# Performance work log

Hardware: AMD Instinct MI355X
Metric: run time of the kernel (lower is better)

## Reference

```python
import jax, jax.numpy as jnp
import numpy as np

V_IN, V_OUT = 128, 128
E_IN, E_OUT = 64, 64
H, L, D = 256, 2, 2
DEC_H = D * L * H  # 1024
S_IN, B, S_OUT = 128, 512, 64


def _lstm_step(h, c, x, W_ih, W_hh, b):
    # PyTorch gate order: i, f, g, o
    gates = x @ W_ih.T + h @ W_hh.T + b
    i, f, g, o = jnp.split(gates, 4, axis=-1)
    c = jax.nn.sigmoid(f) * c + jax.nn.sigmoid(i) * jnp.tanh(g)
    h = jax.nn.sigmoid(o) * jnp.tanh(c)
    return h, c


def _run_lstm_dir(x_seq, W_ih, W_hh, b, reverse):
    # x_seq: [S, B, in]; returns hidden sequence [S, B, H], final (h, c)
    Bsz = x_seq.shape[1]
    Hd = W_hh.shape[1]
    init = (jnp.zeros((Bsz, Hd), x_seq.dtype), jnp.zeros((Bsz, Hd), x_seq.dtype))

    def step(carry, x):
        h, c = _lstm_step(carry[0], carry[1], x, W_ih, W_hh, b)
        return (h, c), h

    (hf, cf), hs = jax.lax.scan(step, init, x_seq, reverse=reverse)
    return hs, hf, cf


def setup_inputs() -> dict:
    key = jax.random.key(0)
    ks = jax.random.split(key, 20)
    s = 0.05
    inp = {}
    inp["input_tokens"] = jax.random.randint(ks[0], (S_IN, B), 0, V_IN, dtype=jnp.int32)
    inp["output_tokens"] = jax.random.randint(ks[1], (B, S_OUT), 0, V_OUT, dtype=jnp.int32)
    inp["in_emb"] = jax.random.normal(ks[2], (V_IN, E_IN), jnp.float32) * s
    # encoder layer 0: input E_IN; layer 1: input D*H. Leading dim 2 = directions.
    inp["enc_W_ih0"] = jax.random.normal(ks[3], (2, 4 * H, E_IN), jnp.float32) * s
    inp["enc_W_hh0"] = jax.random.normal(ks[4], (2, 4 * H, H), jnp.float32) * s
    inp["enc_b0"] = jax.random.normal(ks[5], (2, 4 * H), jnp.float32) * s
    inp["enc_W_ih1"] = jax.random.normal(ks[6], (2, 4 * H, D * H), jnp.float32) * s
    inp["enc_W_hh1"] = jax.random.normal(ks[7], (2, 4 * H, H), jnp.float32) * s
    inp["enc_b1"] = jax.random.normal(ks[8], (2, 4 * H), jnp.float32) * s
    inp["out_emb"] = jax.random.normal(ks[9], (V_OUT, E_OUT), jnp.float32) * s
    inp["dec_W_ih"] = jax.random.normal(ks[10], (4 * DEC_H, E_OUT), jnp.float32) * s
    inp["dec_W_hh"] = jax.random.normal(ks[11], (4 * DEC_H, DEC_H), jnp.float32) * s
    inp["dec_b"] = jax.random.normal(ks[12], (4 * DEC_H,), jnp.float32) * s
    inp["proj_W"] = jax.random.normal(ks[13], (V_OUT, DEC_H), jnp.float32) * s
    inp["proj_b"] = jax.random.normal(ks[14], (V_OUT,), jnp.float32) * s
    return inp


def reference(input_tokens, output_tokens, in_emb,
              enc_W_ih0, enc_W_hh0, enc_b0,
              enc_W_ih1, enc_W_hh1, enc_b1,
              out_emb, dec_W_ih, dec_W_hh, dec_b, proj_W, proj_b):
    # ---- encoder: 2-layer bidirectional LSTM over [S_in, B] ----
    x = in_emb[input_tokens]  # [S, B, E_IN]
    h_list, c_list = [], []
    for W_ih, W_hh, b in ((enc_W_ih0, enc_W_hh0, enc_b0),
                          (enc_W_ih1, enc_W_hh1, enc_b1)):
        hs_f, hf, cf = _run_lstm_dir(x, W_ih[0], W_hh[0], b[0], False)
        hs_b, hb, cb = _run_lstm_dir(x, W_ih[1], W_hh[1], b[1], True)
        x = jnp.concatenate([hs_f, hs_b], axis=-1)  # [S, B, 2H]
        h_list += [hf, hb]
        c_list += [cf, cb]
    Bsz = x.shape[1]
    # PyTorch h_n order: (l0_fwd, l0_bwd, l1_fwd, l1_bwd) -> swapaxes+reshape
    h0 = jnp.stack(h_list, axis=1).reshape(Bsz, -1)  # [B, D*L*H]
    c0 = jnp.stack(c_list, axis=1).reshape(Bsz, -1)

    # ---- decoder: teacher-forced LSTMCell loop ----
    tok_in = output_tokens[:, :-1].T   # [T-1, B]
    tok_next = output_tokens[:, 1:].T  # [T-1, B]

    def step(carry, toks):
        h, c = carry
        t_in, t_next = toks
        e = out_emb[t_in]                                 # [B, E_OUT]
        h, c = _lstm_step(h, c, e, dec_W_ih, dec_W_hh, dec_b)
        logits = c @ proj_W.T + proj_b                    # NOTE: proj on CELL, as in source
        greedy = jnp.argmax(logits, axis=1)
        lp = jax.nn.log_softmax(logits, axis=-1)
        logp = jnp.take_along_axis(lp, t_next[:, None], axis=1)[:, 0]
        return (h, c), (greedy, logp)

    _, (decoded_tokens, log_probs) = jax.lax.scan(step, (h0, c0), (tok_in, tok_next))
    cum_log_probs = jnp.sum(log_probs, axis=0)  # [B]
    return decoded_tokens, cum_log_probs
```

## Files before the change

kernel.cpp:

```cpp
#include <hip/hip_runtime.h>
#include <math.h>

#define B 512
#define S_IN 128
#define S_OUT 64
#define T_DEC 63

#define O_H0   0
#define O_H1   524288
#define O_C    1048576
#define O_BAR  1572864
#define O_HS0  1572868
#define O_P1   (O_HS0 + 33554432)
#define D_HT0  O_HS0
#define D_HT1  (O_HS0 + 524288)
#define D_CT0  (O_HS0 + 1048576)
#define D_CT1  (O_HS0 + 1572864)
#define D_PWT  (O_HS0 + 2097152)

template<int MODE>
__global__ __launch_bounds__(256)
void enc_step(const float* __restrict__ Wih, const float* __restrict__ Whh,
              const float* __restrict__ bias, const int* __restrict__ tok,
              const float* __restrict__ emb, const float* __restrict__ seqin,
              const float* __restrict__ h_in, float* __restrict__ h_out,
              float* __restrict__ c_st, float* __restrict__ seqout,
              const float* __restrict__ p1, int t)
{
    constexpr int KE = (MODE==0) ? 64 : (MODE==2 ? 512 : 0);
    constexpr int K  = KE + 256;
    constexpr int NK = K/16;

    const int dir   = blockIdx.z;
    const int t_eff = dir ? (S_IN-1-t) : t;
    const int hseg  = (MODE==0) ? dir*256 : 512 + dir*256;

    const float* Wih_d = Wih + (size_t)dir*1024*KE;
    const float* Whh_d = Whh + (size_t)dir*1024*256;
    const float* b_d   = bias + dir*1024;

    __shared__ float As[16][64];
    __shared__ float Bs[16][64];

    const int tid = threadIdx.x;
    const int bm0 = blockIdx.x*64;
    const int bn0 = blockIdx.y*64;

    const int la_m  = tid >> 2;
    const int la_k  = (tid & 3) << 2;
    const int a_row = bm0 + la_m;

    const int lb_n = tid >> 2;
    const int lb_k = (tid & 3) << 2;
    const int n_g  = bn0 + lb_n;
    const int b_j  = (n_g & 3)*256 + (n_g >> 2);

    int tokidx = 0;
    if (MODE==0) tokidx = tok[t_eff*B + a_row];

    const int tm = (tid >> 4) << 2;
    const int tn = (tid & 15) << 2;

    float acc[4][4] = {};

    auto loadA = [&](int kt) -> float4 {
        int k = kt*16 + la_k;
        if (MODE==0) {
            if (k < 64) return *(const float4*)&emb[(size_t)tokidx*64 + k];
            return *(const float4*)&h_in[(size_t)a_row*1024 + hseg + (k-64)];
        } else if (MODE==2) {
            if (k < 512) return *(const float4*)&seqin[((size_t)t_eff*B + a_row)*512 + k];
            return *(const float4*)&h_in[(size_t)a_row*1024 + hseg + (k-512)];
        } else {
            return *(const float4*)&h_in[(size_t)a_row*1024 + hseg + k];
        }
    };
    auto loadB = [&](int kt) -> float4 {
        int k = kt*16 + lb_k;
        if (KE && k < KE) return *(const float4*)&Wih_d[(size_t)b_j*KE + k];
        return *(const float4*)&Whh_d[(size_t)b_j*256 + (k-KE)];
    };

    float4 aR = loadA(0), bR = loadB(0);
    for (int kt=0; kt<NK; ++kt) {
        __syncthreads();
        As[la_k+0][la_m]=aR.x; As[la_k+1][la_m]=aR.y; As[la_k+2][la_m]=aR.z; As[la_k+3][la_m]=aR.w;
        Bs[lb_k+0][lb_n]=bR.x; Bs[lb_k+1][lb_n]=bR.y; Bs[lb_k+2][lb_n]=bR.z; Bs[lb_k+3][lb_n]=bR.w;
        __syncthreads();
        if (kt+1 < NK) { aR = loadA(kt+1); bR = loadB(kt+1); }
        #pragma unroll
        for (int k=0;k<16;k++){
            const float4 a = *(const float4*)&As[k][tm];
            const float4 b = *(const float4*)&Bs[k][tn];
            acc[0][0]+=a.x*b.x; acc[0][1]+=a.x*b.y; acc[0][2]+=a.x*b.z; acc[0][3]+=a.x*b.w;
            acc[1][0]+=a.y*b.x; acc[1][1]+=a.y*b.y; acc[1][2]+=a.y*b.z; acc[1][3]+=a.y*b.w;
            acc[2][0]+=a.z*b.x; acc[2][1]+=a.z*b.y; acc[2][2]+=a.z*b.z; acc[2][3]+=a.z*b.w;
            acc[3][0]+=a.w*b.x; acc[3][1]+=a.w*b.y; acc[3][2]+=a.w*b.z; acc[3][3]+=a.w*b.w;
        }
    }

    const int jh = (bn0 + tn) >> 2;
    const float bi = b_d[0*256 + jh];
    const float bf = b_d[1*256 + jh];
    const float bg = b_d[2*256 + jh];
    const float bo = b_d[3*256 + jh];
    #pragma unroll
    for (int i=0;i<4;i++){
        const int brow = bm0 + tm + i;
        float xi = acc[i][0] + bi;
        float xf = acc[i][1] + bf;
        float xg = acc[i][2] + bg;
        float xo = acc[i][3] + bo;
        if (MODE==1) {
            const float4 pv = *(const float4*)&p1[((size_t)dir*512 + brow)*1024 + bn0 + tn];
            xi += pv.x; xf += pv.y; xg += pv.z; xo += pv.w;
        }
        float ig = 1.f/(1.f+expf(-xi));
        float fg = 1.f/(1.f+expf(-xf));
        float gg = tanhf(xg);
        float og = 1.f/(1.f+expf(-xo));
        size_t ci = (size_t)brow*1024 + hseg + jh;
        float cn = fg*c_st[ci] + ig*gg;
        float hn = og*tanhf(cn);
        c_st[ci]  = cn;
        h_out[ci] = hn;
        if (MODE==0) seqout[((size_t)t_eff*B + brow)*512 + dir*256 + jh] = hn;
    }
}

__global__ __launch_bounds__(128)
void gemm_p1(const float* __restrict__ Wih, const float* __restrict__ hs0,
             float* __restrict__ p1out, int s0)
{
    constexpr int NK = 512/16;
    const int dir = blockIdx.z;

    __shared__ float As[16][64];
    __shared__ float Bs[16][64];

    const int tid = threadIdx.x;
    const int bm0 = blockIdx.x*64;
    const int bn0 = blockIdx.y*64;

    const int la_m  = tid >> 1;
    const int la_k  = (tid & 1) << 3;
    const int a_row = bm0 + la_m;

    const int srel  = blockIdx.x >> 3;
    const int sabs  = s0 + srel;
    const int t_eff = dir ? (S_IN-1-sabs) : sabs;
    const int a_b   = a_row & 511;

    const int n_g = bn0 + la_m;
    const int b_j = (n_g & 3)*256 + (n_g >> 2);

    const float* Wih_d = Wih + (size_t)dir*1024*512;

    const int tm = (tid >> 3) << 2;
    const int tn = (tid & 7) << 3;

    float acc[4][8] = {};

    auto loadA = [&](int kt, int q) -> float4 {
        int k = kt*16 + la_k + q*4;
        return *(const float4*)&hs0[((size_t)t_eff*B + a_b)*512 + k];
    };
    auto loadB = [&](int kt, int q) -> float4 {
        int k = kt*16 + la_k + q*4;
        return *(const float4*)&Wih_d[(size_t)b_j*512 + k];
    };

    float4 aR0 = loadA(0,0), aR1 = loadA(0,1);
    float4 bR0 = loadB(0,0), bR1 = loadB(0,1);
    for (int kt=0; kt<NK; ++kt) {
        __syncthreads();
        As[la_k+0][la_m]=aR0.x; As[la_k+1][la_m]=aR0.y; As[la_k+2][la_m]=aR0.z; As[la_k+3][la_m]=aR0.w;
        As[la_k+4][la_m]=aR1.x; As[la_k+5][la_m]=aR1.y; As[la_k+6][la_m]=aR1.z; As[la_k+7][la_m]=aR1.w;
        Bs[la_k+0][la_m]=bR0.x; Bs[la_k+1][la_m]=bR0.y; Bs[la_k+2][la_m]=bR0.z; Bs[la_k+3][la_m]=bR0.w;
        Bs[la_k+4][la_m]=bR1.x; Bs[la_k+5][la_m]=bR1.y; Bs[la_k+6][la_m]=bR1.z; Bs[la_k+7][la_m]=bR1.w;
        __syncthreads();
        if (kt+1 < NK) {
            aR0 = loadA(kt+1,0); aR1 = loadA(kt+1,1);
            bR0 = loadB(kt+1,0); bR1 = loadB(kt+1,1);
        }
        #pragma unroll
        for (int k=0;k<16;k++){
            const float4 a  = *(const float4*)&As[k][tm];
            const float4 b0 = *(const float4*)&Bs[k][tn];
            const float4 b1 = *(const float4*)&Bs[k][tn+4];
            acc[0][0]+=a.x*b0.x; acc[0][1]+=a.x*b0.y; acc[0][2]+=a.x*b0.z; acc[0][3]+=a.x*b0.w;
            acc[0][4]+=a.x*b1.x; acc[0][5]+=a.x*b1.y; acc[0][6]+=a.x*b1.z; acc[0][7]+=a.x*b1.w;
            acc[1][0]+=a.y*b0.x; acc[1][1]+=a.y*b0.y; acc[1][2]+=a.y*b0.z; acc[1][3]+=a.y*b0.w;
            acc[1][4]+=a.y*b1.x; acc[1][5]+=a.y*b1.y; acc[1][6]+=a.y*b1.z; acc[1][7]+=a.y*b1.w;
            acc[2][0]+=a.z*b0.x; acc[2][1]+=a.z*b0.y; acc[2][2]+=a.z*b0.z; acc[2][3]+=a.z*b0.w;
            acc[2][4]+=a.z*b1.x; acc[2][5]+=a.z*b1.y; acc[2][6]+=a.z*b1.z; acc[2][7]+=a.z*b1.w;
            acc[3][0]+=a.w*b0.x; acc[3][1]+=a.w*b0.y; acc[3][2]+=a.w*b0.z; acc[3][3]+=a.w*b0.w;
            acc[3][4]+=a.w*b1.x; acc[3][5]+=a.w*b1.y; acc[3][6]+=a.w*b1.z; acc[3][7]+=a.w*b1.w;
        }
    }

    #pragma unroll
    for (int i=0;i<4;i++){
        const int r = bm0 + tm + i;
        size_t base = ((size_t)(srel*2 + dir)*512 + (r & 511))*1024 + bn0 + tn;
        *(float4*)&p1out[base]   = *(float4*)&acc[i][0];
        *(float4*)&p1out[base+4] = *(float4*)&acc[i][4];
    }
}

__device__ __forceinline__ void grid_bar2(unsigned* cnt, unsigned t)
{
    __syncthreads();
    if (threadIdx.x == 0) {
        __threadfence();
        __hip_atomic_fetch_add(cnt, 1u, __ATOMIC_RELAXED, __HIP_MEMORY_SCOPE_AGENT);
        const unsigned tgt1 = (2u*t + 1u) * 256u;
        while (__hip_atomic_load(cnt, __ATOMIC_RELAXED, __HIP_MEMORY_SCOPE_AGENT) < tgt1)
            __builtin_amdgcn_s_sleep(2);
        __threadfence();
        __hip_atomic_fetch_add(cnt, 1u, __ATOMIC_RELAXED, __HIP_MEMORY_SCOPE_AGENT);
        const unsigned tgt2 = (2u*t + 2u) * 256u;
        while (__hip_atomic_load(cnt, __ATOMIC_RELAXED, __HIP_MEMORY_SCOPE_AGENT) < tgt2)
            __builtin_amdgcn_s_sleep(2);
    }
    __syncthreads();
}

__device__ __forceinline__ void fma4(float* ac, float s, float4 v)
{
    ac[0] += s*v.x; ac[1] += s*v.y; ac[2] += s*v.z; ac[3] += s*v.w;
}

__global__ void prep_kernel(const float* __restrict__ h0, const float* __restrict__ c0,
                            const float* __restrict__ pW, float* __restrict__ hT0,
                            float* __restrict__ cT1, float* __restrict__ pwt)
{
    const int i = blockIdx.x*blockDim.x + threadIdx.x;
    if (i < 524288) {
        const int u = i >> 9, r = i & 511;
        hT0[i] = h0[(size_t)r*1024 + u];
        cT1[i] = c0[(size_t)r*1024 + u];
    }
    if (i < 131072) {
        const int k = i >> 7, v = i & 127;
        pwt[i] = pW[(size_t)v*1024 + k];
    }
}

__global__ __launch_bounds__(1024)
void dec_persist(const float* __restrict__ Wih, const float* __restrict__ Whh,
                 const float* __restrict__ bias, const int* __restrict__ tok,
                 const float* __restrict__ emb, const float* __restrict__ pwt,
                 const float* __restrict__ pb, float* __restrict__ hT0,
                 float* __restrict__ hT1, float* __restrict__ cT0,
                 float* __restrict__ cT1, unsigned* __restrict__ bar,
                 float* __restrict__ dout)
{
    extern __shared__ float smem[];
    float* Ws = smem;
    float* As = smem + 17408;
    float* cs0  = As;
    float* cs1  = As + 1024;
    float* part = As + 2048;
    float* ls   = As + 4096;

    const int b = blockIdx.x, tid = threadIdx.x;
    const int bn0 = b*16;

    {
        const int col = tid >> 6;
        const int n_g = bn0 + col;
        const int wrow = (n_g & 3)*1024 + (n_g >> 2);
        for (int k0 = (tid & 63)*4; k0 < 1088; k0 += 256) {
            float4 v;
            if (k0 < 64) v = *(const float4*)&Wih[(size_t)wrow*64 + k0];
            else         v = *(const float4*)&Whh[(size_t)wrow*1024 + (k0-64)];
            Ws[(k0+0)*16 + col] = v.x;
            Ws[(k0+1)*16 + col] = v.y;
            Ws[(k0+2)*16 + col] = v.z;
            Ws[(k0+3)*16 + col] = v.w;
        }
    }
    __syncthreads();

    const int m   = tid & 511;
    const int tn  = (tid >> 9) << 3;
    const int jh  = (bn0 + tn) >> 2;
    const float bi0 = bias[jh],   bf0 = bias[1024+jh],   bg0 = bias[2048+jh],   bo0 = bias[3072+jh];
    const float bi1 = bias[jh+1], bf1 = bias[1024+jh+1], bg1 = bias[2048+jh+1], bo1 = bias[3072+jh+1];
    const int sj  = tid >> 6;
    const int sr  = (tid & 63)*8;
    const int esm = tid >> 1, esq = tid & 1;

    for (int t = 0; t < T_DEC; ++t) {
        const float* hT_in  = (t & 1) ? hT1 : hT0;
        float*       hT_out = (t & 1) ? hT0 : hT1;
        const float* cT_in  = (t & 1) ? cT0 : cT1;
        float*       cT_out = (t & 1) ? cT1 : cT0;

        const int etok = tok[esm*S_OUT + t];

        float4 pre0 = *(const float4*)&emb[(size_t)etok*64 + esq*8];
        float4 pre1 = *(const float4*)&emb[(size_t)etok*64 + esq*8 + 4];
        float acc[8] = {};

        for (int kt = 0; kt < 68; ++kt) {
            float* buf = As + (kt & 1)*8192;
            if (kt < 4) {
                const int j0 = esq*8;
                buf[(j0+0)*512+esm]=pre0.x; buf[(j0+1)*512+esm]=pre0.y;
                buf[(j0+2)*512+esm]=pre0.z; buf[(j0+3)*512+esm]=pre0.w;
                buf[(j0+4)*512+esm]=pre1.x; buf[(j0+5)*512+esm]=pre1.y;
                buf[(j0+6)*512+esm]=pre1.z; buf[(j0+7)*512+esm]=pre1.w;
            } else {
                *(float4*)&buf[sj*512 + sr]     = pre0;
                *(float4*)&buf[sj*512 + sr + 4] = pre1;
            }
            if (kt+1 < 68) {
                if (kt+1 < 4) {
                    pre0 = *(const float4*)&emb[(size_t)etok*64 + (kt+1)*16 + esq*8];
                    pre1 = *(const float4*)&emb[(size_t)etok*64 + (kt+1)*16 + esq*8 + 4];
                } else {
                    const float* src = &hT_in[(size_t)((kt+1)*16 - 64 + sj)*512 + sr];
                    pre0 = *(const float4*)&src[0];
                    pre1 = *(const float4*)&src[4];
                }
            }
            __syncthreads();
            const int kg = kt*16;
            #pragma unroll
            for (int kk=0;kk<16;kk++){
                const float4 w0 = *(const float4*)&Ws[(kg+kk)*16 + tn];
                const float4 w1 = *(const float4*)&Ws[(kg+kk)*16 + tn + 4];
                const float a  = buf[kk*512 + m];
                fma4(acc+0, a, w0);
                fma4(acc+4, a, w1);
            }
        }

        {
            float xi=acc[0]+bi0, xf=acc[1]+bf0, xg=acc[2]+bg0, xo=acc[3]+bo0;
            float ig=1.f/(1.f+expf(-xi)), fg=1.f/(1.f+expf(-xf));
            float gg=tanhf(xg), og=1.f/(1.f+expf(-xo));
            const size_t ci = (size_t)jh*512 + m;
            const float cn = fg*cT_in[ci] + ig*gg, hn = og*tanhf(cn);
            cT_out[ci] = cn; hT_out[ci] = hn;
        }
        {
            float xi=acc[4]+bi1, xf=acc[5]+bf1, xg=acc[6]+bg1, xo=acc[7]+bo1;
            float ig=1.f/(1.f+expf(-xi)), fg=1.f/(1.f+expf(-xf));
            float gg=tanhf(xg), og=1.f/(1.f+expf(-xo));
            const size_t ci = (size_t)(jh+1)*512 + m;
            const float cn = fg*cT_in[ci] + ig*gg, hn = og*tanhf(cn);
            cT_out[ci] = cn; hT_out[ci] = hn;
        }

        grid_bar2(bar, (unsigned)t);

        {
            const float2 v = *(const float2*)&cT_out[(size_t)tid*512 + 2*b];
            cs0[tid] = v.x; cs1[tid] = v.y;
        }
        __syncthreads();
        {
            const int kgp = tid >> 7, pc = tid & 127;
            float a0 = 0.f, a1 = 0.f;
            const int k0 = kgp*128;
            #pragma unroll 4
            for (int ki=0; ki<128; ++ki){
                const float w = pwt[(size_t)(k0+ki)*128 + pc];
                a0 += w*cs0[k0+ki];
                a1 += w*cs1[k0+ki];
            }
            part[(kgp*2+0)*128 + pc] = a0;
            part[(kgp*2+1)*128 + pc] = a1;
        }
        __syncthreads();
        if (tid < 256) {
            const int pr = tid >> 7, pc = tid & 127;
            float s = pb[pc];
            #pragma unroll
            for (int kg2=0; kg2<8; ++kg2) s += part[(kg2*2+pr)*128 + pc];
            ls[pr*128 + pc] = s;
        }
        __syncthreads();
        if (tid < 128) {
            const int r = tid >> 6, lane = tid & 63;
            const int gb = 2*b + r;
            const float v0 = ls[r*128 + lane], v1 = ls[r*128 + lane + 64];
            float mv; int mi;
            if (v1 > v0){ mv=v1; mi=lane+64; } else { mv=v0; mi=lane; }
            #pragma unroll
            for (int o=32;o>=1;o>>=1){
                const float ov = __shfl_xor(mv, o);
                const int   oi = __shfl_xor(mi, o);
                if (ov > mv || (ov == mv && oi < mi)){ mv=ov; mi=oi; }
            }
            float e = expf(v0-mv) + expf(v1-mv);
            #pragma unroll
            for (int o=32;o>=1;o>>=1) e += __shfl_xor(e, o);
            if (lane == 0){
                const int tnx = tok[gb*S_OUT + t + 1];
                const float logp = ls[r*128 + tnx] - mv - logf(e);
                const float cn = ((t==0)?0.f:dout[T_DEC*B + gb]) + logp;
                dout[T_DEC*B + gb] = cn;
                dout[t*B + gb] = (float)mi;
            }
        }
        __syncthreads();
    }
}

__global__ void zero_kernel(float* __restrict__ p, int n4){
    int i = blockIdx.x*blockDim.x + threadIdx.x;
    if (i < n4) *(float4*)&p[i*4] = float4{0.f,0.f,0.f,0.f};
}

extern "C" void kernel_launch(void* const* d_in, const int* in_sizes, int n_in,
                              void* d_out, int out_size, void* d_ws, size_t ws_size,
                              hipStream_t stream)
{
    const int*   input_tokens  = (const int*)d_in[0];
    const int*   output_tokens = (const int*)d_in[1];
    const float* in_emb  = (const float*)d_in[2];
    const float* eWih0   = (const float*)d_in[3];
    const float* eWhh0   = (const float*)d_in[4];
    const float* eb0     = (const float*)d_in[5];
    const float* eWih1   = (const float*)d_in[6];
    const float* eWhh1   = (const float*)d_in[7];
    const float* eb1     = (const float*)d_in[8];
    const float* out_emb = (const float*)d_in[9];
    const float* dWih    = (const float*)d_in[10];
    const float* dWhh    = (const float*)d_in[11];
    const float* db      = (const float*)d_in[12];
    const float* pW      = (const float*)d_in[13];
    const float* pb      = (const float*)d_in[14];

    size_t ws_fl = ws_size / 4;
    if (ws_fl < (size_t)O_P1) return;

    int CH = 0;
    if      (ws_fl >= (size_t)O_P1 + 16u*1048576u) CH = 16;
    else if (ws_fl >= (size_t)O_P1 +  8u*1048576u) CH = 8;
    else if (ws_fl >= (size_t)O_P1 +  4u*1048576u) CH = 4;
    else if (ws_fl >= (size_t)O_P1 +  2u*1048576u) CH = 2;

    float* ws   = (float*)d_ws;
    float* dout = (float*)d_out;

    float* h[2]   = { ws + O_H0, ws + O_H1 };
    float* c      = ws + O_C;
    unsigned* bar = (unsigned*)(ws + O_BAR);
    float* hs0    = ws + O_HS0;
    float* p1     = ws + O_P1;
    float* hT0    = ws + D_HT0;
    float* hT1    = ws + D_HT1;
    float* cT0    = ws + D_CT0;
    float* cT1    = ws + D_CT1;
    float* pwt    = ws + D_PWT;

    zero_kernel<<<(O_HS0/4 + 255)/256, 256, 0, stream>>>(ws, O_HS0/4);

    for (int t=0;t<S_IN;t++)
        enc_step<0><<<dim3(8,16,2),256,0,stream>>>(eWih0, eWhh0, eb0,
            input_tokens, in_emb, nullptr, h[t&1], h[(t+1)&1], c, hs0, nullptr, t);

    if (CH) {
        for (int s0=0; s0<S_IN; s0+=CH) {
            gemm_p1<<<dim3(CH*8,16,2),128,0,stream>>>(eWih1, hs0, p1, s0);
            for (int s=s0; s<s0+CH; ++s)
                enc_step<1><<<dim3(8,16,2),256,0,stream>>>(eWih1, eWhh1, eb1,
                    nullptr, nullptr, nullptr, h[s&1], h[(s+1)&1], c, nullptr,
                    p1 + (size_t)(s-s0)*2*512*1024, s);
        }
    } else {
        for (int t=0;t<S_IN;t++)
            enc_step<2><<<dim3(8,16,2),256,0,stream>>>(eWih1, eWhh1, eb1,
                nullptr, nullptr, hs0, h[t&1], h[(t+1)&1], c, nullptr, nullptr, t);
    }

    prep_kernel<<<2048,256,0,stream>>>(h[0], c, pW, hT0, cT1, pwt);

    dec_persist<<<256, 1024, 135168, stream>>>(dWih, dWhh, db, output_tokens,
                                               out_emb, pwt, pb, hT0, hT1,
                                               cT0, cT1, bar, dout);
}
```

Before: 17.26 ms.

## Replace per-step encoder launches with persistent grid-barrier kernels keeping weights in LDS

The encoder's 256+ per-timestep kernel launches and the chunked input-projection GEMM are replaced by two persistent kernels, one per layer. Each block keeps its slice of the input and recurrent weights resident in shared memory and loops over all timesteps, synchronising through a global grid barrier. Hidden and cell state are stored transposed, so the layout transpose in the prep kernel is no longer needed. This removes launch overhead and repeated weight reloads, at the cost of per-step grid barriers and of folding the layer-1 input projection back into the sequential loop.

```diff
diff --git a/kernel.cpp b/kernel.cpp
--- a/kernel.cpp
+++ b/kernel.cpp
@@ -6,207 +6,14 @@
 #define S_OUT 64
 #define T_DEC 63
 
-#define O_H0   0
-#define O_H1   524288
-#define O_C    1048576
-#define O_BAR  1572864
-#define O_HS0  1572868
-#define O_P1   (O_HS0 + 33554432)
-#define D_HT0  O_HS0
-#define D_HT1  (O_HS0 + 524288)
-#define D_CT0  (O_HS0 + 1048576)
-#define D_CT1  (O_HS0 + 1572864)
-#define D_PWT  (O_HS0 + 2097152)
-
-template<int MODE>
-__global__ __launch_bounds__(256)
-void enc_step(const float* __restrict__ Wih, const float* __restrict__ Whh,
-              const float* __restrict__ bias, const int* __restrict__ tok,
-              const float* __restrict__ emb, const float* __restrict__ seqin,
-              const float* __restrict__ h_in, float* __restrict__ h_out,
-              float* __restrict__ c_st, float* __restrict__ seqout,
-              const float* __restrict__ p1, int t)
-{
-    constexpr int KE = (MODE==0) ? 64 : (MODE==2 ? 512 : 0);
-    constexpr int K  = KE + 256;
-    constexpr int NK = K/16;
-
-    const int dir   = blockIdx.z;
-    const int t_eff = dir ? (S_IN-1-t) : t;
-    const int hseg  = (MODE==0) ? dir*256 : 512 + dir*256;
-
-    const float* Wih_d = Wih + (size_t)dir*1024*KE;
-    const float* Whh_d = Whh + (size_t)dir*1024*256;
-    const float* b_d   = bias + dir*1024;
-
-    __shared__ float As[16][64];
-    __shared__ float Bs[16][64];
-
-    const int tid = threadIdx.x;
-    const int bm0 = blockIdx.x*64;
-    const int bn0 = blockIdx.y*64;
-
-    const int la_m  = tid >> 2;
-    const int la_k  = (tid & 3) << 2;
-    const int a_row = bm0 + la_m;
-
-    const int lb_n = tid >> 2;
-    const int lb_k = (tid & 3) << 2;
-    const int n_g  = bn0 + lb_n;
-    const int b_j  = (n_g & 3)*256 + (n_g >> 2);
-
-    int tokidx = 0;
-    if (MODE==0) tokidx = tok[t_eff*B + a_row];
-
-    const int tm = (tid >> 4) << 2;
-    const int tn = (tid & 15) << 2;
-
-    float acc[4][4] = {};
-
-    auto loadA = [&](int kt) -> float4 {
-        int k = kt*16 + la_k;
-        if (MODE==0) {
-            if (k < 64) return *(const float4*)&emb[(size_t)tokidx*64 + k];
-            return *(const float4*)&h_in[(size_t)a_row*1024 + hseg + (k-64)];
-        } else if (MODE==2) {
-            if (k < 512) return *(const float4*)&seqin[((size_t)t_eff*B + a_row)*512 + k];
-            return *(const float4*)&h_in[(size_t)a_row*1024 + hseg + (k-512)];
-        } else {
-            return *(const float4*)&h_in[(size_t)a_row*1024 + hseg + k];
-        }
-    };
-    auto loadB = [&](int kt) -> float4 {
-        int k = kt*16 + lb_k;
-        if (KE && k < KE) return *(const float4*)&Wih_d[(size_t)b_j*KE + k];
-        return *(const float4*)&Whh_d[(size_t)b_j*256 + (k-KE)];
-    };
-
-    float4 aR = loadA(0), bR = loadB(0);
-    for (int kt=0; kt<NK; ++kt) {
-        __syncthreads();
-        As[la_k+0][la_m]=aR.x; As[la_k+1][la_m]=aR.y; As[la_k+2][la_m]=aR.z; As[la_k+3][la_m]=aR.w;
-        Bs[lb_k+0][lb_n]=bR.x; Bs[lb_k+1][lb_n]=bR.y; Bs[lb_k+2][lb_n]=bR.z; Bs[lb_k+3][lb_n]=bR.w;
-        __syncthreads();
-        if (kt+1 < NK) { aR = loadA(kt+1); bR = loadB(kt+1); }
-        #pragma unroll
-        for (int k=0;k<16;k++){
-            const float4 a = *(const float4*)&As[k][tm];
-            const float4 b = *(const float4*)&Bs[k][tn];
-            acc[0][0]+=a.x*b.x; acc[0][1]+=a.x*b.y; acc[0][2]+=a.x*b.z; acc[0][3]+=a.x*b.w;
-            acc[1][0]+=a.y*b.x; acc[1][1]+=a.y*b.y; acc[1][2]+=a.y*b.z; acc[1][3]+=a.y*b.w;
-            acc[2][0]+=a.z*b.x; acc[2][1]+=a.z*b.y; acc[2][2]+=a.z*b.z; acc[2][3]+=a.z*b.w;
-            acc[3][0]+=a.w*b.x; acc[3][1]+=a.w*b.y; acc[3][2]+=a.w*b.z; acc[3][3]+=a.w*b.w;
-        }
-    }
-
-    const int jh = (bn0 + tn) >> 2;
-    const float bi = b_d[0*256 + jh];
-    const float bf = b_d[1*256 + jh];
-    const float bg = b_d[2*256 + jh];
-    const float bo = b_d[3*256 + jh];
-    #pragma unroll
-    for (int i=0;i<4;i++){
-        const int brow = bm0 + tm + i;
-        float xi = acc[i][0] + bi;
-        float xf = acc[i][1] + bf;
-        float xg = acc[i][2] + bg;
-        float xo = acc[i][3] + bo;
-        if (MODE==1) {
-            const float4 pv = *(const float4*)&p1[((size_t)dir*512 + brow)*1024 + bn0 + tn];
-            xi += pv.x; xf += pv.y; xg += pv.z; xo += pv.w;
-        }
-        float ig = 1.f/(1.f+expf(-xi));
-        float fg = 1.f/(1.f+expf(-xf));
-        float gg = tanhf(xg);
-        float og = 1.f/(1.f+expf(-xo));
-        size_t ci = (size_t)brow*1024 + hseg + jh;
-        float cn = fg*c_st[ci] + ig*gg;
-        float hn = og*tanhf(cn);
-        c_st[ci]  = cn;
-        h_out[ci] = hn;
-        if (MODE==0) seqout[((size_t)t_eff*B + brow)*512 + dir*256 + jh] = hn;
-    }
-}
-
-__global__ __launch_bounds__(128)
-void gemm_p1(const float* __restrict__ Wih, const float* __restrict__ hs0,
-             float* __restrict__ p1out, int s0)
-{
-    constexpr int NK = 512/16;
-    const int dir = blockIdx.z;
-
-    __shared__ float As[16][64];
-    __shared__ float Bs[16][64];
-
-    const int tid = threadIdx.x;
-    const int bm0 = blockIdx.x*64;
-    const int bn0 = blockIdx.y*64;
-
-    const int la_m  = tid >> 1;
-    const int la_k  = (tid & 1) << 3;
-    const int a_row = bm0 + la_m;
-
-    const int srel  = blockIdx.x >> 3;
-    const int sabs  = s0 + srel;
-    const int t_eff = dir ? (S_IN-1-sabs) : sabs;
-    const int a_b   = a_row & 511;
-
-    const int n_g = bn0 + la_m;
-    const int b_j = (n_g & 3)*256 + (n_g >> 2);
-
-    const float* Wih_d = Wih + (size_t)dir*1024*512;
-
-    const int tm = (tid >> 3) << 2;
-    const int tn = (tid & 7) << 3;
-
-    float acc[4][8] = {};
-
-    auto loadA = [&](int kt, int q) -> float4 {
-        int k = kt*16 + la_k + q*4;
-        return *(const float4*)&hs0[((size_t)t_eff*B + a_b)*512 + k];
-    };
-    auto loadB = [&](int kt, int q) -> float4 {
-        int k = kt*16 + la_k + q*4;
-        return *(const float4*)&Wih_d[(size_t)b_j*512 + k];
-    };
-
-    float4 aR0 = loadA(0,0), aR1 = loadA(0,1);
-    float4 bR0 = loadB(0,0), bR1 = loadB(0,1);
-    for (int kt=0; kt<NK; ++kt) {
-        __syncthreads();
-        As[la_k+0][la_m]=aR0.x; As[la_k+1][la_m]=aR0.y; As[la_k+2][la_m]=aR0.z; As[la_k+3][la_m]=aR0.w;
-        As[la_k+4][la_m]=aR1.x; As[la_k+5][la_m]=aR1.y; As[la_k+6][la_m]=aR1.z; As[la_k+7][la_m]=aR1.w;
-        Bs[la_k+0][la_m]=bR0.x; Bs[la_k+1][la_m]=bR0.y; Bs[la_k+2][la_m]=bR0.z; Bs[la_k+3][la_m]=bR0.w;
-        Bs[la_k+4][la_m]=bR1.x; Bs[la_k+5][la_m]=bR1.y; Bs[la_k+6][la_m]=bR1.z; Bs[la_k+7][la_m]=bR1.w;
-        __syncthreads();
-        if (kt+1 < NK) {
-            aR0 = loadA(kt+1,0); aR1 = loadA(kt+1,1);
-            bR0 = loadB(kt+1,0); bR1 = loadB(kt+1,1);
-        }
-        #pragma unroll
-        for (int k=0;k<16;k++){
-            const float4 a  = *(const float4*)&As[k][tm];
-            const float4 b0 = *(const float4*)&Bs[k][tn];
-            const float4 b1 = *(const float4*)&Bs[k][tn+4];
-            acc[0][0]+=a.x*b0.x; acc[0][1]+=a.x*b0.y; acc[0][2]+=a.x*b0.z; acc[0][3]+=a.x*b0.w;
-            acc[0][4]+=a.x*b1.x; acc[0][5]+=a.x*b1.y; acc[0][6]+=a.x*b1.z; acc[0][7]+=a.x*b1.w;
-            acc[1][0]+=a.y*b0.x; acc[1][1]+=a.y*b0.y; acc[1][2]+=a.y*b0.z; acc[1][3]+=a.y*b0.w;
-            acc[1][4]+=a.y*b1.x; acc[1][5]+=a.y*b1.y; acc[1][6]+=a.y*b1.z; acc[1][7]+=a.y*b1.w;
-            acc[2][0]+=a.z*b0.x; acc[2][1]+=a.z*b0.y; acc[2][2]+=a.z*b0.z; acc[2][3]+=a.z*b0.w;
-            acc[2][4]+=a.z*b1.x; acc[2][5]+=a.z*b1.y; acc[2][6]+=a.z*b1.z; acc[2][7]+=a.z*b1.w;
-            acc[3][0]+=a.w*b0.x; acc[3][1]+=a.w*b0.y; acc[3][2]+=a.w*b0.z; acc[3][3]+=a.w*b0.w;
-            acc[3][4]+=a.w*b1.x; acc[3][5]+=a.w*b1.y; acc[3][6]+=a.w*b1.z; acc[3][7]+=a.w*b1.w;
-        }
-    }
-
-    #pragma unroll
-    for (int i=0;i<4;i++){
-        const int r = bm0 + tm + i;
-        size_t base = ((size_t)(srel*2 + dir)*512 + (r & 511))*1024 + bn0 + tn;
-        *(float4*)&p1out[base]   = *(float4*)&acc[i][0];
-        *(float4*)&p1out[base+4] = *(float4*)&acc[i][4];
-    }
-}
+#define W_HT0 0
+#define W_HT1 524288
+#define W_CT1 1048576
+#define W_BAR 1572864
+#define W_HS0 1572868
+#define W_CT0 W_HS0
+#define W_PWT (W_HS0 + 524288)
+#define WS_MIN (W_HS0 + 33554432)
 
 __device__ __forceinline__ void grid_bar2(unsigned* cnt, unsigned t)
 {
@@ -231,16 +38,133 @@
     ac[0] += s*v.x; ac[1] += s*v.y; ac[2] += s*v.z; ac[3] += s*v.w;
 }
 
-__global__ void prep_kernel(const float* __restrict__ h0, const float* __restrict__ c0,
-                            const float* __restrict__ pW, float* __restrict__ hT0,
-                            float* __restrict__ cT1, float* __restrict__ pwt)
+template<int L>
+__global__ __launch_bounds__(1024)
+void enc_persist(const float* __restrict__ Wih, const float* __restrict__ Whh,
+                 const float* __restrict__ bias, const int* __restrict__ tok,
+                 const float* __restrict__ emb, const float* __restrict__ hs0,
+                 float* __restrict__ hs0_out, float* __restrict__ hT0,
+                 float* __restrict__ hT1, float* __restrict__ cT,
+                 unsigned* __restrict__ bar)
+{
+    constexpr int KE = (L==0) ? 64 : 512;
+    constexpr int K  = KE + 256;
+    constexpr int NK = K/16;
+    constexpr int WSZ = K*8;
+
+    extern __shared__ float smem[];
+    float* Ws  = smem;
+    float* As  = smem + WSZ;
+
+    const int b = blockIdx.x, tid = threadIdx.x;
+    const int dir = b >> 7;
+    const int up  = (b & 127) * 2;
+
+    const float* Wih_d = Wih + (size_t)dir*1024*KE;
+    const float* Whh_d = Whh + (size_t)dir*1024*256;
+    const float* b_d   = bias + dir*1024;
+
+    {
+        const int lc = tid >> 7;
+        const int q  = tid & 127;
+        const int n  = up*4 + lc;
+        const int j  = (n & 3)*256 + (n >> 2);
+        for (int k0 = q*4; k0 < K; k0 += 512) {
+            float4 v;
+            if (k0 < KE) v = *(const float4*)&Wih_d[(size_t)j*KE + k0];
+            else         v = *(const float4*)&Whh_d[(size_t)j*256 + (k0-KE)];
+            Ws[(k0+0)*8 + lc] = v.x;
+            Ws[(k0+1)*8 + lc] = v.y;
+            Ws[(k0+2)*8 + lc] = v.z;
+            Ws[(k0+3)*8 + lc] = v.w;
+        }
+    }
+    __syncthreads();
+
+    const int m  = tid & 511;
+    const int cg = tid >> 9;
+    const int u  = up + cg;
+    const float bi = b_d[u], bf = b_d[256+u], bg_ = b_d[512+u], bo = b_d[768+u];
+    const int ub   = (L==0) ? dir*256 : 512 + dir*256;
+    const int sj  = tid >> 6;
+    const int sr  = (tid & 63)*8;
+    const int esm = tid >> 1, esq = tid & 1;
+
+    for (int t = 0; t < S_IN; ++t) {
+        const float* hT_in  = (t & 1) ? hT1 : hT0;
+        float*       hT_out = (t & 1) ? hT0 : hT1;
+        const int t_eff = dir ? (S_IN-1-t) : t;
+
+        int etok = 0;
+        if (L==0) etok = tok[t_eff*B + esm];
+
+        float4 pre0, pre1;
+        if (L==0) {
+            pre0 = *(const float4*)&emb[(size_t)etok*64 + esq*8];
+            pre1 = *(const float4*)&emb[(size_t)etok*64 + esq*8 + 4];
+        } else {
+            const float* src = &hs0[((size_t)t_eff*512 + sj)*512 + sr];
+            pre0 = *(const float4*)&src[0];
+            pre1 = *(const float4*)&src[4];
+        }
+        float acc[4] = {};
+
+        for (int kt = 0; kt < NK; ++kt) {
+            float* buf = As + (kt & 1)*8192;
+            if (L==0 && kt < 4) {
+                const int j0 = esq*8;
+                buf[(j0+0)*512+esm]=pre0.x; buf[(j0+1)*512+esm]=pre0.y;
+                buf[(j0+2)*512+esm]=pre0.z; buf[(j0+3)*512+esm]=pre0.w;
+                buf[(j0+4)*512+esm]=pre1.x; buf[(j0+5)*512+esm]=pre1.y;
+                buf[(j0+6)*512+esm]=pre1.z; buf[(j0+7)*512+esm]=pre1.w;
+            } else {
+                *(float4*)&buf[sj*512 + sr]     = pre0;
+                *(float4*)&buf[sj*512 + sr + 4] = pre1;
+            }
+            if (kt+1 < NK) {
+                const int kb = (kt+1)*16;
+                if (L==0 && kt+1 < 4) {
+                    pre0 = *(const float4*)&emb[(size_t)etok*64 + kb + esq*8];
+                    pre1 = *(const float4*)&emb[(size_t)etok*64 + kb + esq*8 + 4];
+                } else if (L==1 && kt+1 < 32) {
+                    const float* src = &hs0[((size_t)t_eff*512 + kb + sj)*512 + sr];
+                    pre0 = *(const float4*)&src[0];
+                    pre1 = *(const float4*)&src[4];
+                } else {
+                    const float* src = &hT_in[(size_t)(ub + kb - KE + sj)*512 + sr];
+                    pre0 = *(const float4*)&src[0];
+                    pre1 = *(const float4*)&src[4];
+                }
+            }
+            __syncthreads();
+            const int kg = kt*16;
+            #pragma unroll
+            for (int kk=0;kk<16;kk++){
+                const float4 w = *(const float4*)&Ws[(kg+kk)*8 + cg*4];
+                const float a  = buf[kk*512 + m];
+                fma4(acc, a, w);
+            }
+        }
+
+        {
+            float xi=acc[0]+bi, xf=acc[1]+bf, xg=acc[2]+bg_, xo=acc[3]+bo;
+            float ig=1.f/(1.f+expf(-xi)), fg=1.f/(1.f+expf(-xf));
+            float gg=tanhf(xg), og=1.f/(1.f+expf(-xo));
+            const size_t ci = (size_t)(ub + u)*512 + m;
+            const float cn = fg*cT[ci] + ig*gg;
+            const float hn = og*tanhf(cn);
+            cT[ci] = cn; hT_out[ci] = hn;
+            if (L==0)
+                hs0_out[((size_t)t_eff*512 + dir*256 + u)*512 + m] = hn;
+        }
+
+        grid_bar2(bar, (unsigned)t);
+    }
+}
+
+__global__ void prep_kernel(const float* __restrict__ pW, float* __restrict__ pwt)
 {
     const int i = blockIdx.x*blockDim.x + threadIdx.x;
-    if (i < 524288) {
-        const int u = i >> 9, r = i & 511;
-        hT0[i] = h0[(size_t)r*1024 + u];
-        cT1[i] = c0[(size_t)r*1024 + u];
-    }
     if (i < 131072) {
         const int k = i >> 7, v = i & 127;
         pwt[i] = pW[(size_t)v*1024 + k];
@@ -436,52 +360,32 @@
     const float* pW      = (const float*)d_in[13];
     const float* pb      = (const float*)d_in[14];
 
-    size_t ws_fl = ws_size / 4;
-    if (ws_fl < (size_t)O_P1) return;
-
-    int CH = 0;
-    if      (ws_fl >= (size_t)O_P1 + 16u*1048576u) CH = 16;
-    else if (ws_fl >= (size_t)O_P1 +  8u*1048576u) CH = 8;
-    else if (ws_fl >= (size_t)O_P1 +  4u*1048576u) CH = 4;
-    else if (ws_fl >= (size_t)O_P1 +  2u*1048576u) CH = 2;
+    if (ws_size < (size_t)WS_MIN * 4) return;
 
     float* ws   = (float*)d_ws;
     float* dout = (float*)d_out;
 
-    float* h[2]   = { ws + O_H0, ws + O_H1 };
-    float* c      = ws + O_C;
-    unsigned* bar = (unsigned*)(ws + O_BAR);
-    float* hs0    = ws + O_HS0;
-    float* p1     = ws + O_P1;
-    float* hT0    = ws + D_HT0;
-    float* hT1    = ws + D_HT1;
-    float* cT0    = ws + D_CT0;
-    float* cT1    = ws + D_CT1;
-    float* pwt    = ws + D_PWT;
-
-    zero_kernel<<<(O_HS0/4 + 255)/256, 256, 0, stream>>>(ws, O_HS0/4);
-
-    for (int t=0;t<S_IN;t++)
-        enc_step<0><<<dim3(8,16,2),256,0,stream>>>(eWih0, eWhh0, eb0,
-            input_tokens, in_emb, nullptr, h[t&1], h[(t+1)&1], c, hs0, nullptr, t);
-
-    if (CH) {
-        for (int s0=0; s0<S_IN; s0+=CH) {
-            gemm_p1<<<dim3(CH*8,16,2),128,0,stream>>>(eWih1, hs0, p1, s0);
-            for (int s=s0; s<s0+CH; ++s)
-                enc_step<1><<<dim3(8,16,2),256,0,stream>>>(eWih1, eWhh1, eb1,
-                    nullptr, nullptr, nullptr, h[s&1], h[(s+1)&1], c, nullptr,
-                    p1 + (size_t)(s-s0)*2*512*1024, s);
-        }
-    } else {
-        for (int t=0;t<S_IN;t++)
-            enc_step<2><<<dim3(8,16,2),256,0,stream>>>(eWih1, eWhh1, eb1,
-                nullptr, nullptr, hs0, h[t&1], h[(t+1)&1], c, nullptr, nullptr, t);
-    }
-
-    prep_kernel<<<2048,256,0,stream>>>(h[0], c, pW, hT0, cT1, pwt);
+    float* hT0    = ws + W_HT0;
+    float* hT1    = ws + W_HT1;
+    float* cT1    = ws + W_CT1;
+    unsigned* bar = (unsigned*)(ws + W_BAR);
+    float* hs0    = ws + W_HS0;
+    float* cT0    = ws + W_CT0;
+    float* pwt    = ws + W_PWT;
+
+    zero_kernel<<<(W_HS0/4 + 255)/256, 256, 0, stream>>>(ws, W_HS0/4);
+
+    enc_persist<0><<<256, 1024, (320*8 + 2*8192)*4, stream>>>(
+        eWih0, eWhh0, eb0, input_tokens, in_emb, nullptr, hs0,
+        hT0, hT1, cT1, bar + 0);
+
+    enc_persist<1><<<256, 1024, (768*8 + 2*8192)*4, stream>>>(
+        eWih1, eWhh1, eb1, nullptr, nullptr, hs0, nullptr,
+        hT0, hT1, cT1, bar + 1);
+
+    prep_kernel<<<512, 256, 0, stream>>>(pW, pwt);
 
     dec_persist<<<256, 1024, 135168, stream>>>(dWih, dWhh, db, output_tokens,
                                                out_emb, pwt, pb, hT0, hT1,
-                                               cT0, cT1, bar, dout);
-}
+                                               cT0, cT1, bar + 2, dout);
+}
```

Result: slower. 26.26 ms (+52.1%).
